# Performance work log

Hardware: AMD Instinct MI355X
Metric: run time of the kernel (lower is better)

## Reference

```python
import jax, jax.numpy as jnp
import numpy as np

D_MODEL = 1024
D_FF = 4096
NUM_HEADS = 16
D_HEAD = D_MODEL // NUM_HEADS
EPS = 1e-5


def setup_inputs() -> dict:
    key = jax.random.key(0)
    ks = jax.random.split(key, 16)
    s = 0.02
    return {
        "X": jax.random.normal(ks[0], (2, 2048, D_MODEL), dtype=jnp.float32),
        "W_qkv": jax.random.normal(ks[1], (D_MODEL, 3 * D_MODEL), dtype=jnp.float32) * s,
        "b_qkv": jax.random.normal(ks[2], (3 * D_MODEL,), dtype=jnp.float32) * s,
        "W_o": jax.random.normal(ks[3], (D_MODEL, D_MODEL), dtype=jnp.float32) * s,
        "b_o": jax.random.normal(ks[4], (D_MODEL,), dtype=jnp.float32) * s,
        "W_1": jax.random.normal(ks[5], (D_MODEL, D_FF), dtype=jnp.float32) * s,
        "b_1": jax.random.normal(ks[6], (D_FF,), dtype=jnp.float32) * s,
        "W_2": jax.random.normal(ks[7], (D_FF, D_MODEL), dtype=jnp.float32) * s,
        "b_2": jax.random.normal(ks[8], (D_MODEL,), dtype=jnp.float32) * s,
        "ln1_g": jnp.ones((D_MODEL,), dtype=jnp.float32),
        "ln1_b": jnp.zeros((D_MODEL,), dtype=jnp.float32),
        "ln2_g": jnp.ones((D_MODEL,), dtype=jnp.float32),
        "ln2_b": jnp.zeros((D_MODEL,), dtype=jnp.float32),
    }


def _layernorm(x, g, b):
    mu = jnp.mean(x, axis=-1, keepdims=True)
    var = jnp.mean(jnp.square(x - mu), axis=-1, keepdims=True)
    return (x - mu) * jax.lax.rsqrt(var + EPS) * g + b


def reference(X, W_qkv, b_qkv, W_o, b_o, W_1, b_1, W_2, b_2, ln1_g, ln1_b, ln2_g, ln2_b):
    B, T, D = X.shape
    qkv = X @ W_qkv + b_qkv                      # [B,T,3D]
    Q, K, V = jnp.split(qkv, 3, axis=-1)
    # [B,H,T,d]
    Q = Q.reshape(B, T, NUM_HEADS, D_HEAD).transpose(0, 2, 1, 3)
    K = K.reshape(B, T, NUM_HEADS, D_HEAD).transpose(0, 2, 1, 3)
    V = V.reshape(B, T, NUM_HEADS, D_HEAD).transpose(0, 2, 1, 3)
    scores = jnp.einsum('bhqd,bhkd->bhqk', Q, K) / np.float32(D_HEAD) ** 0.5
    causal = jnp.tril(jnp.ones((T, T), dtype=bool))
    scores = jnp.where(causal, scores, jnp.float32(-jnp.inf))
    A = jax.nn.softmax(scores, axis=-1)
    O = jnp.einsum('bhqk,bhkd->bhqd', A, V)
    O = O.transpose(0, 2, 1, 3).reshape(B, T, D)
    O = O @ W_o + b_o
    H_1 = _layernorm(X + O, ln1_g, ln1_b)
    H_2 = (jax.nn.gelu(H_1 @ W_1 + b_1, approximate=False)) @ W_2 + b_2
    return _layernorm(H_1 + H_2, ln2_g, ln2_b)
```

## Files before the change

### kernel.cpp

```cpp
#include <hip/hip_runtime.h>
#include <cmath>

typedef unsigned short u16;
typedef __bf16 bf16x8 __attribute__((ext_vector_type(8)));
typedef float f32x4 __attribute__((ext_vector_type(4)));

#define DEVI __device__ __forceinline__

DEVI float b2f(u16 u){ union{unsigned int i; float f;} v; v.i=(unsigned int)u<<16; return v.f; }
DEVI u16 f2b(float f){ union{unsigned int i; float f;} v; v.f=f;
    unsigned int r=(v.i+0x7FFFu+((v.i>>16)&1u))>>16; return (u16)r; }

DEVI void gload_lds16(const u16* g, u16* l){
    __builtin_amdgcn_global_load_lds((__attribute__((address_space(1))) void*)g,
                                     (__attribute__((address_space(3))) void*)l,
                                     16, 0, 0);
}

__global__ __launch_bounds__(256)
void cvt_bf16(const float* __restrict__ in, u16* __restrict__ out)
{
    const int i = (blockIdx.x * 256 + threadIdx.x) * 4;
    float4 v = *(const float4*)&in[i];
    ushort4 o;
    o.x = f2b(v.x); o.y = f2b(v.y); o.z = f2b(v.z); o.w = f2b(v.w);
    *(ushort4*)&out[i] = o;
}

__global__ __launch_bounds__(256)
void cvt_transpose(const float* __restrict__ in, u16* __restrict__ out, int R, int C)
{
    __shared__ __align__(16) u16 tile[64*72];
    const int rb = blockIdx.x*64, cb = blockIdx.y*64;
    const int t = threadIdx.x;
    const int r = t >> 3, c0 = (t & 7) * 8;
    #pragma unroll
    for (int rr = 0; rr < 2; rr++) {
        const int row = r + rr*32;
        float4 a = *(const float4*)&in[(long)(rb + row)*C + cb + c0];
        float4 b = *(const float4*)&in[(long)(rb + row)*C + cb + c0 + 4];
        u16* tp = &tile[row*72 + c0];
        tp[0]=f2b(a.x); tp[1]=f2b(a.y); tp[2]=f2b(a.z); tp[3]=f2b(a.w);
        tp[4]=f2b(b.x); tp[5]=f2b(b.y); tp[6]=f2b(b.z); tp[7]=f2b(b.w);
    }
    __syncthreads();
    #pragma unroll
    for (int rr = 0; rr < 2; rr++) {
        const int cr = r + rr*32;
        u16 tmp[8];
        #pragma unroll
        for (int j = 0; j < 8; j++) tmp[j] = tile[(c0 + j)*72 + cr];
        *(uint4*)&out[(long)(cb + cr)*R + rb + c0] = *(uint4*)tmp;
    }
}

template<int EPI, int BM>
__global__ __launch_bounds__(256)
void gemm_bt(const u16* __restrict__ A, const u16* __restrict__ Bt,
             const float* __restrict__ bias, const u16* __restrict__ Res,
             u16* __restrict__ C, u16* __restrict__ C2, int M, int N, int K)
{
    constexpr int RM = BM / 32;
    constexpr int NA = (BM / 16) * 2 / 4;
    __shared__ __align__(16) u16 As[BM*64];
    __shared__ __align__(16) u16 Bs[128*64];
    const int tid  = threadIdx.x;
    const int wave = tid >> 6, lane = tid & 63;
    const int tm = blockIdx.x * BM, tn = blockIdx.y * 128;

    const int rs = lane >> 2, cs = (lane & 3) * 8;
    const u16* gA[NA]; u16* lA[NA];
    #pragma unroll
    for (int i = 0; i < NA; i++) {
        const int c = wave + i*4;
        const int p = c / (BM/16), rb = c % (BM/16);
        gA[i] = A + (long)(tm + rb*16 + rs)*K + p*32 + cs;
        lA[i] = As + p*(BM*32) + rb*512;
    }
    const u16* gB[4]; u16* lB[4];
    #pragma unroll
    for (int i = 0; i < 4; i++) {
        const int c = wave + i*4;
        const int p = c >> 3, rb = c & 7;
        gB[i] = Bt + (long)(tn + rb*16 + rs)*K + p*32 + cs;
        lB[i] = Bs + p*(128*32) + rb*512;
    }

    const int wm = (wave >> 1) * (BM/2), wn = (wave & 1) * 64;
    const int fr = lane & 15, fq = lane >> 4;

    f32x4 acc[RM][4] = {};
    for (int k0 = 0; k0 < K; k0 += 64) {
        __syncthreads();
        #pragma unroll
        for (int i = 0; i < NA; i++) gload_lds16(gA[i] + k0, lA[i]);
        #pragma unroll
        for (int i = 0; i < 4; i++)  gload_lds16(gB[i] + k0, lB[i]);
        __syncthreads();
        #pragma unroll
        for (int p = 0; p < 2; p++) {
            bf16x8 af[RM], bfr[4];
            #pragma unroll
            for (int i = 0; i < RM; i++)
                af[i]  = *(const bf16x8*)&As[p*(BM*32) + (wm + i*16 + fr)*32 + fq*8];
            #pragma unroll
            for (int j = 0; j < 4; j++)
                bfr[j] = *(const bf16x8*)&Bs[p*(128*32) + (wn + j*16 + fr)*32 + fq*8];
            #pragma unroll
            for (int i = 0; i < RM; i++)
                #pragma unroll
                for (int j = 0; j < 4; j++)
                    acc[i][j] = __builtin_amdgcn_mfma_f32_16x16x32_bf16(af[i], bfr[j], acc[i][j], 0, 0, 0);
        }
    }

    #pragma unroll
    for (int i = 0; i < RM; i++) {
        const int row = tm + wm + i*16 + fq*4;
        #pragma unroll
        for (int j = 0; j < 4; j++) {
            const int col = tn + wn + j*16 + fr;
            const float bv = bias[col];
            if (EPI == 3 && col >= 2048) {
                const int hh = (col - 2048) >> 6, dd = (col - 2048) & 63;
                const int batch = row >> 11, tok = row & 2047;
                u16 pk[4];
                #pragma unroll
                for (int r = 0; r < 4; r++) pk[r] = f2b(acc[i][j][r] + bv);
                *(uint2*)&C2[((long)(batch*16 + hh)*64 + dd)*2048 + tok] = *(uint2*)pk;
            } else {
                const int cw = (EPI == 3) ? 2048 : N;
                #pragma unroll
                for (int r = 0; r < 4; r++) {
                    float v = acc[i][j][r] + bv;
                    const long idx = (long)(row + r)*cw + col;
                    if (EPI == 1) v += b2f(Res[idx]);
                    if (EPI == 2) {
                        const float u = v + 0.044715f*v*v*v;
                        const float t = exp2f(u * 2.302208f);
                        v = v * t * __builtin_amdgcn_rcpf(t + 1.f);
                    }
                    C[idx] = f2b(v);
                }
            }
        }
    }
}

__global__ __launch_bounds__(256)
void attn_kernel(const u16* __restrict__ QK, const u16* __restrict__ VT,
                 u16* __restrict__ O)
{
    constexpr float CS = 0.18033688011112042f;
    __shared__ __align__(16) u16 Ks[2][4096];
    __shared__ __align__(16) u16 Vs[2][4096];
    __shared__ __align__(16) u16 Ps[4][1024];

    const int tid = threadIdx.x, wave = tid >> 6, lane = tid & 63;
    const int pair = blockIdx.x, h = blockIdx.y, b = blockIdx.z;
    const int fr = lane & 15, fq = lane >> 4;
    const long qkbase = (long)b*2048*2048;
    const long vtbase = (long)(b*16 + h)*64*2048;
    const int rs = lane >> 2, cs2 = (lane & 3) * 8;
    const int sw = (fr & 7) * 8;

    #define ISSUE(bf, k0)                                                      \
        _Pragma("unroll")                                                      \
        for (int i = 0; i < 2; i++) {                                          \
            const int c = wave + i*4;                                          \
            const int kp = c >> 2, krb = c & 3;                                \
            gload_lds16(QK + qkbase + (long)((k0) + krb*16 + rs)*2048          \
                           + 1024 + h*64 + kp*32 + cs2,                        \
                        &Ks[bf][kp*2048 + krb*512]);                           \
            const int vp = c & 1, vrb = c >> 1;                                \
            gload_lds16(VT + vtbase + (long)(vrb*16 + rs)*2048                 \
                           + (k0) + vp*32 + cs2,                               \
                        &Vs[bf][vp*2048 + vrb*512]);                           \
        }

    #pragma unroll 1
    for (int which = 0; which < 2; which++) {
        const int qt = which ? pair : (31 - pair);

        bf16x8 bq[2];
        #pragma unroll
        for (int ks = 0; ks < 2; ks++)
            bq[ks] = *(const bf16x8*)&QK[qkbase + (long)(qt*64 + wave*16 + fr)*2048
                                         + h*64 + ks*32 + fq*8];

        const int q_glob = qt*64 + wave*16 + fr;
        const int q_wmin = qt*64 + wave*16;
        f32x4 o[4] = {};
        float m_i = -1e30f, l_i = 0.f;
        const int nkt = qt + 1;

        if (which) __syncthreads();
        ISSUE(0, 0)

        for (int kt = 0; kt < nkt; kt++) {
            const int k0 = kt * 64;
            const int cur = kt & 1;
            __syncthreads();
            if (kt + 1 < nkt) { ISSUE(cur ^ 1, k0 + 64) }

            f32x4 st[4];
            #pragma unroll
            for (int mt = 0; mt < 4; mt++) st[mt] = (f32x4){0.f,0.f,0.f,0.f};
            #pragma unroll
            for (int mt = 0; mt < 4; mt++)
                #pragma unroll
                for (int ks = 0; ks < 2; ks++) {
                    bf16x8 ak = *(const bf16x8*)&Ks[cur][ks*2048 + (mt*16 + fr)*32 + fq*8];
                    st[mt] = __builtin_amdgcn_mfma_f32_16x16x32_bf16(ak, bq[ks], st[mt], 0, 0, 0);
                }

            float mx = -1e30f;
            if (k0 + 63 > q_wmin) {
                #pragma unroll
                for (int mt = 0; mt < 4; mt++)
                    #pragma unroll
                    for (int r = 0; r < 4; r++) {
                        const int key = k0 + mt*16 + fq*4 + r;
                        float v = st[mt][r];
                        if (key > q_glob) v = -1e30f;
                        st[mt][r] = v;
                        mx = fmaxf(mx, v);
                    }
            } else {
                #pragma unroll
                for (int mt = 0; mt < 4; mt++)
                    #pragma unroll
                    for (int r = 0; r < 4; r++) mx = fmaxf(mx, st[mt][r]);
            }
            mx = fmaxf(mx, __shfl_xor(mx, 16, 64));
            mx = fmaxf(mx, __shfl_xor(mx, 32, 64));

            if (mx > m_i + 44.357f) {
                const float alpha = exp2f((m_i - mx) * CS);
                #pragma unroll
                for (int dt = 0; dt < 4; dt++)
                    #pragma unroll
                    for (int r = 0; r < 4; r++) o[dt][r] *= alpha;
                l_i *= alpha;
                m_i = mx;
            }
            const float nms = -m_i * CS;
            float ps = 0.f;
            #pragma unroll
            for (int mt = 0; mt < 4; mt++)
                #pragma unroll
                for (int r = 0; r < 4; r++) {
                    const float p = exp2f(fmaf(st[mt][r], CS, nms));
                    st[mt][r] = p; ps += p;
                }
            ps += __shfl_xor(ps, 16, 64);
            ps += __shfl_xor(ps, 32, 64);
            l_i += ps;

            u16* pw = Ps[wave];
            #pragma unroll
            for (int mt = 0; mt < 4; mt++)
                #pragma unroll
                for (int d = 0; d < 2; d++) {
                    unsigned pk;
                    asm("v_cvt_pk_bf16_f32 %0, %1, %2"
                        : "=v"(pk) : "v"(st[mt][2*d]), "v"(st[mt][2*d+1]));
                    *(unsigned*)&pw[fr*64 + ((mt*16 + fq*4 + 2*d) ^ sw)] = pk;
                }
            __asm__ volatile("" ::: "memory");
            bf16x8 bp[2];
            #pragma unroll
            for (int kk = 0; kk < 2; kk++)
                bp[kk] = *(const bf16x8*)&pw[fr*64 + ((kk*32 + fq*8) ^ sw)];
            #pragma unroll
            for (int dt = 0; dt < 4; dt++)
                #pragma unroll
                for (int kk = 0; kk < 2; kk++) {
                    bf16x8 av = *(const bf16x8*)&Vs[cur][kk*2048 + (dt*16 + fr)*32 + fq*8];
                    o[dt] = __builtin_amdgcn_mfma_f32_16x16x32_bf16(av, bp[kk], o[dt], 0, 0, 0);
                }
            __asm__ volatile("" ::: "memory");
        }

        const float rl = __builtin_amdgcn_rcpf(l_i);
        const long orow = (long)b*2048 + qt*64 + wave*16 + fr;
        #pragma unroll
        for (int dt = 0; dt < 4; dt++) {
            u16 pk[4];
            #pragma unroll
            for (int r = 0; r < 4; r++) pk[r] = f2b(o[dt][r] * rl);
            *(uint2*)&O[orow*1024 + h*64 + dt*16 + fq*4] = *(uint2*)pk;
        }
    }
    #undef ISSUE
}

template<int OUTF32>
__global__ __launch_bounds__(256)
void ln_kernel(const u16* __restrict__ X, const float* __restrict__ G,
               const float* __restrict__ B, void* __restrict__ Yv)
{
    __shared__ float red[8];
    const int tid = threadIdx.x;
    const long row = blockIdx.x;
    const u16* x = X + row*1024;
    ushort4 u = *(const ushort4*)&x[tid*4];
    const float v0 = b2f(u.x), v1 = b2f(u.y), v2 = b2f(u.z), v3 = b2f(u.w);
    float s = v0+v1+v2+v3;
    float q = v0*v0+v1*v1+v2*v2+v3*v3;
    #pragma unroll
    for (int off = 32; off >= 1; off >>= 1) {
        s += __shfl_xor(s, off, 64);
        q += __shfl_xor(q, off, 64);
    }
    const int wv = tid >> 6;
    if ((tid & 63) == 0) { red[wv*2] = s; red[wv*2+1] = q; }
    __syncthreads();
    s = red[0]+red[2]+red[4]+red[6];
    q = red[1]+red[3]+red[5]+red[7];
    const float mu = s * (1.f/1024.f);
    const float rstd = rsqrtf(fmaxf(q*(1.f/1024.f) - mu*mu, 0.f) + 1e-5f);
    float4 g4 = *(const float4*)&G[tid*4];
    float4 b4 = *(const float4*)&B[tid*4];
    const float y0 = (v0-mu)*rstd*g4.x + b4.x;
    const float y1 = (v1-mu)*rstd*g4.y + b4.y;
    const float y2 = (v2-mu)*rstd*g4.z + b4.z;
    const float y3 = (v3-mu)*rstd*g4.w + b4.w;
    if (OUTF32) {
        float4 o = make_float4(y0, y1, y2, y3);
        *(float4*)&((float*)Yv)[row*1024 + tid*4] = o;
    } else {
        ushort4 o;
        o.x = f2b(y0); o.y = f2b(y1); o.z = f2b(y2); o.w = f2b(y3);
        *(ushort4*)&((u16*)Yv)[row*1024 + tid*4] = o;
    }
}

extern "C" void kernel_launch(void* const* d_in, const int* in_sizes, int n_in,
                              void* d_out, int out_size, void* d_ws, size_t ws_size,
                              hipStream_t stream)
{
    const float* X    = (const float*)d_in[0];
    const float* Wqkv = (const float*)d_in[1];
    const float* bqkv = (const float*)d_in[2];
    const float* Wo   = (const float*)d_in[3];
    const float* bo   = (const float*)d_in[4];
    const float* W1   = (const float*)d_in[5];
    const float* b1   = (const float*)d_in[6];
    const float* W2   = (const float*)d_in[7];
    const float* b2   = (const float*)d_in[8];
    const float* g1   = (const float*)d_in[9];
    const float* be1  = (const float*)d_in[10];
    const float* g2   = (const float*)d_in[11];
    const float* be2  = (const float*)d_in[12];
    float* out = (float*)d_out;

    char* ws = (char*)d_ws;
    u16* Xbf   = (u16*)(ws + 0);
    u16* WqkvT = (u16*)(ws + 8388608);
    u16* WoT   = (u16*)(ws + 14680064);
    u16* QK    = (u16*)(ws + 16777216);
    u16* VT    = (u16*)(ws + 33554432);
    u16* AO    = (u16*)(ws + 41943040);
    u16* S1    = (u16*)(ws + 16777216);
    u16* H1    = (u16*)(ws + 0);
    u16* Gbuf  = (u16*)(ws + 8388608);
    u16* S2    = (u16*)(ws + 41943040);
    u16* W1T   = (u16*)d_out;
    u16* W2T   = (u16*)d_out + 4194304;

    cvt_bf16<<<4096, 256, 0, stream>>>(X, Xbf);
    cvt_transpose<<<dim3(16, 48), 256, 0, stream>>>(Wqkv, WqkvT, 1024, 3072);
    cvt_transpose<<<dim3(16, 16), 256, 0, stream>>>(Wo,   WoT,   1024, 1024);
    cvt_transpose<<<dim3(16, 64), 256, 0, stream>>>(W1,   W1T,   1024, 4096);
    cvt_transpose<<<dim3(64, 16), 256, 0, stream>>>(W2,   W2T,   4096, 1024);

    gemm_bt<3,128><<<dim3(32, 24), 256, 0, stream>>>(Xbf, WqkvT, bqkv, nullptr, QK, VT, 4096, 3072, 1024);
    attn_kernel<<<dim3(16, 16, 2), 256, 0, stream>>>(QK, VT, AO);
    gemm_bt<1,64><<<dim3(64, 8), 256, 0, stream>>>(AO, WoT, bo, Xbf, S1, nullptr, 4096, 1024, 1024);
    ln_kernel<0><<<4096, 256, 0, stream>>>(S1, g1, be1, H1);
    gemm_bt<2,128><<<dim3(32, 32), 256, 0, stream>>>(H1, W1T, b1, nullptr, Gbuf, nullptr, 4096, 4096, 1024);
    gemm_bt<1,64><<<dim3(64, 8), 256, 0, stream>>>(Gbuf, W2T, b2, H1, S2, nullptr, 4096, 1024, 4096);
    ln_kernel<1><<<4096, 256, 0, stream>>>(S2, g2, be2, out);
}
```

Baseline: 364.5 us.

## Split attention KV loop across two wave groups with in-block softmax merge

Attention blocks grow from 256 to 512 threads. Two wave groups each process alternate key tiles for the same 64 query rows, with their own double-buffered K/V in LDS. Their partial (m, l, O) states are merged through shared memory at the end. This halves the serial KV-loop length per block to hide latency and raise parallelism, at the cost of more LDS, extra barriers and a merge step.

```diff
diff --git a/kernel.cpp b/kernel.cpp
--- a/kernel.cpp
+++ b/kernel.cpp
@@ -147,35 +147,37 @@
     }
 }
 
-__global__ __launch_bounds__(256)
+__global__ __launch_bounds__(512)
 void attn_kernel(const u16* __restrict__ QK, const u16* __restrict__ VT,
                  u16* __restrict__ O)
 {
     constexpr float CS = 0.18033688011112042f;
-    __shared__ __align__(16) u16 Ks[2][4096];
-    __shared__ __align__(16) u16 Vs[2][4096];
-    __shared__ __align__(16) u16 Ps[4][1024];
+    __shared__ __align__(16) u16 smem[40960];
 
     const int tid = threadIdx.x, wave = tid >> 6, lane = tid & 63;
+    const int grp = wave >> 2, wg = wave & 3;
     const int pair = blockIdx.x, h = blockIdx.y, b = blockIdx.z;
     const int fr = lane & 15, fq = lane >> 4;
     const long qkbase = (long)b*2048*2048;
     const long vtbase = (long)(b*16 + h)*64*2048;
     const int rs = lane >> 2, cs2 = (lane & 3) * 8;
     const int sw = (fr & 7) * 8;
+    const int KsBase = grp*8192;
+    const int VsBase = 16384 + grp*8192;
+    u16* pw = &smem[32768 + wave*1024];
 
     #define ISSUE(bf, k0)                                                      \
         _Pragma("unroll")                                                      \
         for (int i = 0; i < 2; i++) {                                          \
-            const int c = wave + i*4;                                          \
+            const int c = wg + i*4;                                            \
             const int kp = c >> 2, krb = c & 3;                                \
             gload_lds16(QK + qkbase + (long)((k0) + krb*16 + rs)*2048          \
                            + 1024 + h*64 + kp*32 + cs2,                        \
-                        &Ks[bf][kp*2048 + krb*512]);                           \
+                        &smem[KsBase + (bf)*4096 + kp*2048 + krb*512]);        \
             const int vp = c & 1, vrb = c >> 1;                                \
             gload_lds16(VT + vtbase + (long)(vrb*16 + rs)*2048                 \
                            + (k0) + vp*32 + cs2,                               \
-                        &Vs[bf][vp*2048 + vrb*512]);                           \
+                        &smem[VsBase + (bf)*4096 + vp*2048 + vrb*512]);        \
         }
 
     #pragma unroll 1
@@ -185,111 +187,137 @@
         bf16x8 bq[2];
         #pragma unroll
         for (int ks = 0; ks < 2; ks++)
-            bq[ks] = *(const bf16x8*)&QK[qkbase + (long)(qt*64 + wave*16 + fr)*2048
+            bq[ks] = *(const bf16x8*)&QK[qkbase + (long)(qt*64 + wg*16 + fr)*2048
                                          + h*64 + ks*32 + fq*8];
 
-        const int q_glob = qt*64 + wave*16 + fr;
-        const int q_wmin = qt*64 + wave*16;
+        const int q_glob = qt*64 + wg*16 + fr;
+        const int q_wmin = qt*64 + wg*16;
         f32x4 o[4] = {};
         float m_i = -1e30f, l_i = 0.f;
         const int nkt = qt + 1;
+        const int nit = (nkt + 1) >> 1;
+        const int myn = (nkt + 1 - grp) >> 1;
 
         if (which) __syncthreads();
-        ISSUE(0, 0)
-
-        for (int kt = 0; kt < nkt; kt++) {
+        if (grp < nkt) { ISSUE(0, grp*64) }
+
+        for (int it = 0; it < nit; it++) {
+            const int kt = 2*it + grp;
             const int k0 = kt * 64;
-            const int cur = kt & 1;
+            const int cur = it & 1;
             __syncthreads();
-            if (kt + 1 < nkt) { ISSUE(cur ^ 1, k0 + 64) }
-
-            f32x4 st[4];
-            #pragma unroll
-            for (int mt = 0; mt < 4; mt++) st[mt] = (f32x4){0.f,0.f,0.f,0.f};
-            #pragma unroll
-            for (int mt = 0; mt < 4; mt++)
-                #pragma unroll
-                for (int ks = 0; ks < 2; ks++) {
-                    bf16x8 ak = *(const bf16x8*)&Ks[cur][ks*2048 + (mt*16 + fr)*32 + fq*8];
-                    st[mt] = __builtin_amdgcn_mfma_f32_16x16x32_bf16(ak, bq[ks], st[mt], 0, 0, 0);
+            if (kt + 2 < nkt) { ISSUE(cur ^ 1, k0 + 128) }
+
+            if (it < myn) {
+                f32x4 st[4];
+                #pragma unroll
+                for (int mt = 0; mt < 4; mt++) st[mt] = (f32x4){0.f,0.f,0.f,0.f};
+                #pragma unroll
+                for (int mt = 0; mt < 4; mt++)
+                    #pragma unroll
+                    for (int ks = 0; ks < 2; ks++) {
+                        bf16x8 ak = *(const bf16x8*)&smem[KsBase + cur*4096 + ks*2048 + (mt*16 + fr)*32 + fq*8];
+                        st[mt] = __builtin_amdgcn_mfma_f32_16x16x32_bf16(ak, bq[ks], st[mt], 0, 0, 0);
+                    }
+
+                float mx = -1e30f;
+                if (k0 + 63 > q_wmin) {
+                    #pragma unroll
+                    for (int mt = 0; mt < 4; mt++)
+                        #pragma unroll
+                        for (int r = 0; r < 4; r++) {
+                            const int key = k0 + mt*16 + fq*4 + r;
+                            float v = st[mt][r];
+                            if (key > q_glob) v = -1e30f;
+                            st[mt][r] = v;
+                            mx = fmaxf(mx, v);
+                        }
+                } else {
+                    #pragma unroll
+                    for (int mt = 0; mt < 4; mt++)
+                        #pragma unroll
+                        for (int r = 0; r < 4; r++) mx = fmaxf(mx, st[mt][r]);
                 }
-
-            float mx = -1e30f;
-            if (k0 + 63 > q_wmin) {
+                mx = fmaxf(mx, __shfl_xor(mx, 16, 64));
+                mx = fmaxf(mx, __shfl_xor(mx, 32, 64));
+
+                if (mx > m_i + 44.357f) {
+                    const float alpha = exp2f((m_i - mx) * CS);
+                    #pragma unroll
+                    for (int dt = 0; dt < 4; dt++)
+                        #pragma unroll
+                        for (int r = 0; r < 4; r++) o[dt][r] *= alpha;
+                    l_i *= alpha;
+                    m_i = mx;
+                }
+                const float nms = -m_i * CS;
+                float ps = 0.f;
                 #pragma unroll
                 for (int mt = 0; mt < 4; mt++)
                     #pragma unroll
                     for (int r = 0; r < 4; r++) {
-                        const int key = k0 + mt*16 + fq*4 + r;
-                        float v = st[mt][r];
-                        if (key > q_glob) v = -1e30f;
-                        st[mt][r] = v;
-                        mx = fmaxf(mx, v);
+                        const float p = exp2f(fmaf(st[mt][r], CS, nms));
+                        st[mt][r] = p; ps += p;
                     }
-            } else {
+                ps += __shfl_xor(ps, 16, 64);
+                ps += __shfl_xor(ps, 32, 64);
+                l_i += ps;
+
                 #pragma unroll
                 for (int mt = 0; mt < 4; mt++)
                     #pragma unroll
-                    for (int r = 0; r < 4; r++) mx = fmaxf(mx, st[mt][r]);
+                    for (int d = 0; d < 2; d++) {
+                        unsigned pk;
+                        asm("v_cvt_pk_bf16_f32 %0, %1, %2"
+                            : "=v"(pk) : "v"(st[mt][2*d]), "v"(st[mt][2*d+1]));
+                        *(unsigned*)&pw[fr*64 + ((mt*16 + fq*4 + 2*d) ^ sw)] = pk;
+                    }
+                __asm__ volatile("" ::: "memory");
+                bf16x8 bp[2];
+                #pragma unroll
+                for (int kk = 0; kk < 2; kk++)
+                    bp[kk] = *(const bf16x8*)&pw[fr*64 + ((kk*32 + fq*8) ^ sw)];
+                #pragma unroll
+                for (int dt = 0; dt < 4; dt++)
+                    #pragma unroll
+                    for (int kk = 0; kk < 2; kk++) {
+                        bf16x8 av = *(const bf16x8*)&smem[VsBase + cur*4096 + kk*2048 + (dt*16 + fr)*32 + fq*8];
+                        o[dt] = __builtin_amdgcn_mfma_f32_16x16x32_bf16(av, bp[kk], o[dt], 0, 0, 0);
+                    }
+                __asm__ volatile("" ::: "memory");
             }
-            mx = fmaxf(mx, __shfl_xor(mx, 16, 64));
-            mx = fmaxf(mx, __shfl_xor(mx, 32, 64));
-
-            if (mx > m_i + 44.357f) {
-                const float alpha = exp2f((m_i - mx) * CS);
-                #pragma unroll
-                for (int dt = 0; dt < 4; dt++)
-                    #pragma unroll
-                    for (int r = 0; r < 4; r++) o[dt][r] *= alpha;
-                l_i *= alpha;
-                m_i = mx;
-            }
-            const float nms = -m_i * CS;
-            float ps = 0.f;
-            #pragma unroll
-            for (int mt = 0; mt < 4; mt++)
-                #pragma unroll
-                for (int r = 0; r < 4; r++) {
-                    const float p = exp2f(fmaf(st[mt][r], CS, nms));
-                    st[mt][r] = p; ps += p;
-                }
-            ps += __shfl_xor(ps, 16, 64);
-            ps += __shfl_xor(ps, 32, 64);
-            l_i += ps;
-
-            u16* pw = Ps[wave];
-            #pragma unroll
-            for (int mt = 0; mt < 4; mt++)
-                #pragma unroll
-                for (int d = 0; d < 2; d++) {
-                    unsigned pk;
-                    asm("v_cvt_pk_bf16_f32 %0, %1, %2"
-                        : "=v"(pk) : "v"(st[mt][2*d]), "v"(st[mt][2*d+1]));
-                    *(unsigned*)&pw[fr*64 + ((mt*16 + fq*4 + 2*d) ^ sw)] = pk;
-                }
-            __asm__ volatile("" ::: "memory");
-            bf16x8 bp[2];
-            #pragma unroll
-            for (int kk = 0; kk < 2; kk++)
-                bp[kk] = *(const bf16x8*)&pw[fr*64 + ((kk*32 + fq*8) ^ sw)];
+        }
+
+        __syncthreads();
+        float* MB = (float*)&smem[8192];
+        float* ML = (float*)&smem[24576];
+        if (grp == 1) {
             #pragma unroll
             for (int dt = 0; dt < 4; dt++)
-                #pragma unroll
-                for (int kk = 0; kk < 2; kk++) {
-                    bf16x8 av = *(const bf16x8*)&Vs[cur][kk*2048 + (dt*16 + fr)*32 + fq*8];
-                    o[dt] = __builtin_amdgcn_mfma_f32_16x16x32_bf16(av, bp[kk], o[dt], 0, 0, 0);
-                }
-            __asm__ volatile("" ::: "memory");
-        }
-
-        const float rl = __builtin_amdgcn_rcpf(l_i);
-        const long orow = (long)b*2048 + qt*64 + wave*16 + fr;
-        #pragma unroll
-        for (int dt = 0; dt < 4; dt++) {
-            u16 pk[4];
+                *(f32x4*)&MB[(wg*64 + lane)*16 + dt*4] = o[dt];
+            if (fq == 0) {
+                ML[(wg*16 + fr)*2]     = m_i;
+                ML[(wg*16 + fr)*2 + 1] = l_i;
+            }
+        }
+        __syncthreads();
+        if (grp == 0) {
+            const float m1 = ML[(wg*16 + fr)*2];
+            const float l1 = ML[(wg*16 + fr)*2 + 1];
+            const float m  = fmaxf(m_i, m1);
+            const float e0 = exp2f((m_i - m) * CS);
+            const float e1 = exp2f((m1  - m) * CS);
+            const float rl = __builtin_amdgcn_rcpf(l_i*e0 + l1*e1);
+            const long orow = (long)b*2048 + qt*64 + wg*16 + fr;
             #pragma unroll
-            for (int r = 0; r < 4; r++) pk[r] = f2b(o[dt][r] * rl);
-            *(uint2*)&O[orow*1024 + h*64 + dt*16 + fq*4] = *(uint2*)pk;
+            for (int dt = 0; dt < 4; dt++) {
+                f32x4 o1 = *(const f32x4*)&MB[(wg*64 + lane)*16 + dt*4];
+                u16 pk[4];
+                #pragma unroll
+                for (int r = 0; r < 4; r++)
+                    pk[r] = f2b((o[dt][r]*e0 + o1[r]*e1) * rl);
+                *(uint2*)&O[orow*1024 + h*64 + dt*16 + fq*4] = *(uint2*)pk;
+            }
         }
     }
     #undef ISSUE
@@ -376,7 +404,7 @@
     cvt_transpose<<<dim3(64, 16), 256, 0, stream>>>(W2,   W2T,   4096, 1024);
 
     gemm_bt<3,128><<<dim3(32, 24), 256, 0, stream>>>(Xbf, WqkvT, bqkv, nullptr, QK, VT, 4096, 3072, 1024);
-    attn_kernel<<<dim3(16, 16, 2), 256, 0, stream>>>(QK, VT, AO);
+    attn_kernel<<<dim3(16, 16, 2), 512, 0, stream>>>(QK, VT, AO);
     gemm_bt<1,64><<<dim3(64, 8), 256, 0, stream>>>(AO, WoT, bo, Xbf, S1, nullptr, 4096, 1024, 1024);
     ln_kernel<0><<<4096, 256, 0, stream>>>(S1, g1, be1, H1);
     gemm_bt<2,128><<<dim3(32, 32), 256, 0, stream>>>(H1, W1T, b1, nullptr, Gbuf, nullptr, 4096, 4096, 1024);
```

Result: no change. 364.1 us (-0.1%).
